# Kernel tuning notes

Hardware: AMD Instinct MI355X
Metric: run time of the kernel (lower is better)

The kernel has to match this reference:

```python
import jax, jax.numpy as jnp
import numpy as np

HEADS = 8
DIM_HEAD = 64
DIM = 512
KERNEL = 33
SCALE = DIM_HEAD ** -0.5


def setup_inputs() -> dict:
    key = jax.random.key(0)
    k1, k2, k3, k4, k5, k6 = jax.random.split(key, 6)
    b, n = 2, 2048
    inner = HEADS * DIM_HEAD
    x = jax.random.normal(k1, (b, n, DIM), dtype=jnp.float32)
    mask = jax.random.uniform(k2, (b, n)) < 0.9
    W_qkv = jax.random.normal(k3, (DIM, inner * 3), dtype=jnp.float32) / np.sqrt(DIM)
    W_out = jax.random.normal(k4, (inner, DIM), dtype=jnp.float32) / np.sqrt(inner)
    b_out = jax.random.normal(k5, (DIM,), dtype=jnp.float32) * 0.01
    # depthwise Conv2d(heads, heads, (K,1), groups=heads) weight: (O=heads, I/groups=1, K, 1)
    conv_w = jax.random.normal(k6, (HEADS, 1, KERNEL, 1), dtype=jnp.float32) / np.sqrt(KERNEL)
    return {"x": x, "mask": mask, "W_qkv": W_qkv, "W_out": W_out,
            "b_out": b_out, "conv_w": conv_w}


def reference(x, mask, W_qkv, W_out, b_out, conv_w):
    b, n, _ = x.shape
    h, d = HEADS, DIM_HEAD
    qkv = (x @ W_qkv).reshape(b, n, 3, h, d)          # chunk(3) then (h d) split
    q = qkv[:, :, 0].transpose(0, 2, 1, 3)            # b h n d
    k = qkv[:, :, 1].transpose(0, 2, 1, 3)
    v = qkv[:, :, 2].transpose(0, 2, 1, 3)
    dots = jnp.einsum('bhid,bhjd->bhij', q, k) * SCALE
    mask_value = -jnp.finfo(dots.dtype).max
    dots = jnp.where(mask[:, None, None, :], dots, mask_value)
    attn = jax.nn.softmax(dots, axis=-1)
    out = jnp.einsum('bhij,bhjd->bhid', attn, v)      # b h n d
    # depthwise residual conv over sequence axis (height), per head
    pad = KERNEL // 2
    res = jax.lax.conv_general_dilated(
        v, conv_w, window_strides=(1, 1), padding=((pad, pad), (0, 0)),
        dimension_numbers=('NCHW', 'OIHW', 'NCHW'), feature_group_count=h)
    out = out + res
    out = out.transpose(0, 2, 1, 3).reshape(b, n, h * d)  # b n (h d)
    out = out @ W_out + b_out
    out = jnp.where(mask[:, :, None], out, 0.0)
    return out
```

## Files before the change

kernel.cpp:

```cpp
#include <hip/hip_runtime.h>
#include <float.h>

#define BATCH 2
#define SEQ   2048
#define HEADS 8
#define DHEAD 64
#define DIMM  512
#define NQKV  1536
#define QSCALE_L2 (0.125f * 1.44269504f)

#define QKV_ELEMS ((size_t)BATCH * HEADS * SEQ * DHEAD)
#define BHS (BATCH * HEADS * SEQ)
#define NSPLIT 4

typedef __bf16 bf16x8 __attribute__((ext_vector_type(8)));
typedef short  s16x4  __attribute__((ext_vector_type(4)));
typedef float  f32x4  __attribute__((ext_vector_type(4)));

#if __has_builtin(__builtin_amdgcn_exp2f)
#define EXP2F __builtin_amdgcn_exp2f
#else
#define EXP2F exp2f
#endif

__device__ __forceinline__ unsigned short bfbits(float f) {
  __bf16 h = (__bf16)f;
  return *(unsigned short*)&h;
}
__device__ __forceinline__ float bf2f(unsigned short u) {
  return __uint_as_float((unsigned)u << 16);
}
__device__ __forceinline__ unsigned cvtpk(float a, float b) {
  unsigned r;
  asm("v_cvt_pk_bf16_f32 %0, %1, %2" : "=v"(r) : "v"(a), "v"(b));
  return r;
}
__device__ __forceinline__ f32x4 mfma16(s16x4 a, s16x4 b, f32x4 c) {
#if __has_builtin(__builtin_amdgcn_mfma_f32_16x16x16bf16_1k)
  return __builtin_amdgcn_mfma_f32_16x16x16bf16_1k(a, b, c, 0, 0, 0);
#else
  f32x4 d;
  asm("v_mfma_f32_16x16x16_bf16 %0, %1, %2, %3" : "=v"(d) : "v"(a), "v"(b), "v"(c));
  return d;
#endif
}

__device__ __forceinline__ void transpose_tile_dev(
    const float* __restrict__ W, unsigned short* __restrict__ Wt,
    int K, int N, int n0, int k0, int t, float T[64][65]) {
  {
    int r0 = t >> 4, c4 = t & 15;
#pragma unroll
    for (int rr = 0; rr < 4; ++rr) {
      int r = r0 + rr * 16;
      float4 v = *(const float4*)(W + (size_t)(k0 + r) * N + n0 + c4 * 4);
      T[r][c4 * 4 + 0] = v.x; T[r][c4 * 4 + 1] = v.y;
      T[r][c4 * 4 + 2] = v.z; T[r][c4 * 4 + 3] = v.w;
    }
  }
  __syncthreads();
  {
    int n = t >> 2, kc = t & 3;
    union { unsigned short u[16]; int4 v[2]; } p;
#pragma unroll
    for (int i = 0; i < 16; ++i) p.u[i] = bfbits(T[kc * 16 + i][n]);
    int4* dst = (int4*)(Wt + (size_t)(n0 + n) * K + k0 + kc * 16);
    dst[0] = p.v[0]; dst[1] = p.v[1];
  }
}

__global__ __launch_bounds__(256) void prep_all(
    const float* __restrict__ X, const void* __restrict__ mraw,
    const float* __restrict__ Wqkv, const float* __restrict__ Wout,
    unsigned short* __restrict__ Xbf, float* __restrict__ maskf,
    unsigned short* __restrict__ Wtq, unsigned short* __restrict__ Wto,
    unsigned* __restrict__ kmaxn) {
  __shared__ float T[64][65];
  __shared__ int f_bf16, f_f32, f_gt1, f_oddnz;
  const int b = blockIdx.x;
  const int t = threadIdx.x;
  if (b < 1024) {
    size_t i = ((size_t)b * 256 + t) * 8;
    float4 a0 = *(const float4*)(X + i);
    float4 a1 = *(const float4*)(X + i + 4);
    union { unsigned short u[8]; int4 v; } pk;
    pk.u[0] = bfbits(a0.x); pk.u[1] = bfbits(a0.y);
    pk.u[2] = bfbits(a0.z); pk.u[3] = bfbits(a0.w);
    pk.u[4] = bfbits(a1.x); pk.u[5] = bfbits(a1.y);
    pk.u[6] = bfbits(a1.z); pk.u[7] = bfbits(a1.w);
    *(int4*)(Xbf + i) = pk.v;
  } else if (b < 1216) {
    int bb2 = b - 1024;
    transpose_tile_dev(Wqkv, Wtq, DIMM, NQKV, (bb2 % 24) * 64, (bb2 / 24) * 64, t, T);
  } else if (b < 1280) {
    int bb2 = b - 1216;
    transpose_tile_dev(Wout, Wto, DIMM, DIMM, (bb2 & 7) * 64, (bb2 >> 3) * 64, t, T);
  } else {
    if (t < 16) kmaxn[t] = 0u;
    if (t == 0) { f_bf16 = 0; f_f32 = 0; f_gt1 = 0; f_oddnz = 0; }
    __syncthreads();
    const unsigned int* w = (const unsigned int*)mraw;
    unsigned int v = w[t];
    if (v == 0x3f803f80u) f_bf16 = 1;
    if (v == 0x3f800000u) f_f32 = 1;
    if (v > 1u)           f_gt1 = 1;
    if ((t & 1) && v != 0u) f_oddnz = 1;
    __syncthreads();
    int mode;
    if (f_bf16)       mode = 4;
    else if (f_f32)   mode = 3;
    else if (f_gt1)   mode = 1;
    else if (!f_oddnz) mode = 2;
    else              mode = 0;
    for (int i = t; i < BATCH * SEQ; i += 256) {
      bool keep;
      if (mode == 4)      keep = ((const unsigned short*)mraw)[i] != 0;
      else if (mode == 3) keep = ((const float*)mraw)[i] != 0.f;
      else if (mode == 1) keep = ((const unsigned char*)mraw)[i] != 0;
      else if (mode == 2) keep = w[2 * i] != 0u;
      else                keep = w[i] != 0u;
      maskf[i] = keep ? 1.f : 0.f;
    }
  }
}

__global__ __launch_bounds__(256) void gemm_qkv_mfma(
    const unsigned short* __restrict__ Xbf, const unsigned short* __restrict__ Wt,
    unsigned short* __restrict__ Qbf, unsigned short* __restrict__ Kbf,
    unsigned short* __restrict__ Vt, unsigned* __restrict__ kmaxn) {
  __shared__ __align__(16) unsigned char Al[128 * 128];
  __shared__ __align__(16) unsigned char Bl[64 * 128];
  const int tid = threadIdx.x;
  const int lane = tid & 63;
  const int w = tid >> 6;
  const int l15 = lane & 15, g = lane >> 4;
  const int wr = w >> 1, wc = w & 1;
  int bid = blockIdx.x;
  int lid = (bid & 7) * 96 + (bid >> 3);
  int by = lid / 24, bx = lid - by * 24;
  const int m0 = by * 128;

  f32x4 acc[4][2] = {};
  const int srow = tid >> 3, scg = tid & 7;
  const int rsw = (l15 & 7) << 4;

  for (int k0 = 0; k0 < DIMM; k0 += 64) {
    __syncthreads();
#pragma unroll
    for (int it = 0; it < 4; ++it) {
      int row = srow + it * 32;
      int sw = (row & 7) << 4;
      *(int4*)(Al + row * 128 + ((scg * 16) ^ sw)) =
          *(const int4*)(Xbf + (size_t)(m0 + row) * DIMM + k0 + scg * 8);
      if (it < 2) {
        *(int4*)(Bl + row * 128 + ((scg * 16) ^ sw)) =
            *(const int4*)(Wt + (size_t)(bx * 64 + row) * DIMM + k0 + scg * 8);
      }
    }
    __syncthreads();
#pragma unroll
    for (int ks = 0; ks < 2; ++ks) {
      bf16x8 af[4], bfr[2];
#pragma unroll
      for (int mi = 0; mi < 4; ++mi)
        af[mi] = *(const bf16x8*)(Al + (wr * 64 + mi * 16 + l15) * 128 +
                                  ((ks * 64 + g * 16) ^ rsw));
#pragma unroll
      for (int nj = 0; nj < 2; ++nj)
        bfr[nj] = *(const bf16x8*)(Bl + (wc * 32 + nj * 16 + l15) * 128 +
                                   ((ks * 64 + g * 16) ^ rsw));
#pragma unroll
      for (int mi = 0; mi < 4; ++mi)
#pragma unroll
        for (int nj = 0; nj < 2; ++nj)
          acc[mi][nj] = __builtin_amdgcn_mfma_f32_16x16x32_bf16(
              af[mi], bfr[nj], acc[mi][nj], 0, 0, 0);
    }
  }
  const int chunk = bx >> 3;
  const int bb = m0 >> 11;
  const int hh = bx & 7;
  if (chunk == 2) {
#pragma unroll
    for (int nj = 0; nj < 2; ++nj) {
      int dd = wc * 32 + nj * 16 + l15;
#pragma unroll
      for (int mi = 0; mi < 4; ++mi) {
        int ii0 = (m0 & (SEQ - 1)) + wr * 64 + mi * 16 + g * 4;
        union { unsigned short u[4]; ushort4 v; } pk;
#pragma unroll
        for (int r = 0; r < 4; ++r) pk.u[r] = bfbits(acc[mi][nj][r]);
        *(ushort4*)(Vt + ((size_t)(bb * HEADS + hh) * DHEAD + dd) * SEQ + ii0) = pk.v;
      }
    }
  } else {
    if (chunk == 1) {
      float kab = 0.f;
#pragma unroll
      for (int nj = 0; nj < 2; ++nj)
#pragma unroll
        for (int mi = 0; mi < 4; ++mi)
#pragma unroll
          for (int r = 0; r < 4; ++r) kab = fmaxf(kab, fabsf(acc[mi][nj][r]));
#pragma unroll
      for (int d = 1; d < 64; d <<= 1) kab = fmaxf(kab, __shfl_xor(kab, d));
      if (lane == 0)
        atomicMax(kmaxn + (bb * HEADS + hh), __float_as_uint(kab * 1.005f));
    }
    unsigned short* dst = (chunk == 0) ? Qbf : Kbf;
    const float sc = (chunk == 0) ? QSCALE_L2 : 1.f;
    __syncthreads();
#pragma unroll
    for (int nj = 0; nj < 2; ++nj) {
      int dd = wc * 32 + nj * 16 + l15;
#pragma unroll
      for (int mi = 0; mi < 4; ++mi) {
#pragma unroll
        for (int r = 0; r < 4; ++r) {
          int rowl = wr * 64 + mi * 16 + g * 4 + r;
          *(unsigned short*)(Al + rowl * 128 + ((dd * 2) ^ ((rowl & 7) << 4))) =
              bfbits(acc[mi][nj][r] * sc);
        }
      }
    }
    __syncthreads();
    const int rr = tid >> 1, hf = tid & 1;
    const int ii0 = (m0 & (SEQ - 1));
    unsigned short* gout =
        dst + ((size_t)(bb * HEADS + hh) * SEQ + ii0 + rr) * DHEAD + hf * 32;
    const int sw2 = (rr & 7) << 4;
#pragma unroll
    for (int q = 0; q < 4; ++q)
      *(int4*)(gout + q * 8) =
          *(const int4*)(Al + rr * 128 + ((hf * 64 + q * 16) ^ sw2));
  }
}

__global__ __launch_bounds__(256) void attn_split(const unsigned short* __restrict__ Qbf,
                                                  const unsigned short* __restrict__ Kbf,
                                                  const unsigned short* __restrict__ Vt,
                                                  const float* __restrict__ maskf,
                                                  const unsigned* __restrict__ kmaxn,
                                                  unsigned short* __restrict__ Po,
                                                  float* __restrict__ LSUM) {
  __shared__ __align__(16) unsigned char Ks[16384];
  __shared__ __align__(16) unsigned char Vs[16384];

  const int tid = threadIdx.x;
  const int lane = tid & 63;
  const int w = tid >> 6;
  const int l15 = lane & 15, g = lane >> 4;

  int fid = blockIdx.x;
  int lid = (fid & 7) * 128 + (fid >> 3);
  const int bh = lid >> 6;
  const int rem = lid & 63;
  const int qp = rem >> 2;
  const int quarter = rem & 3;
  const int bb = bh >> 3;

  const unsigned short* Qg = Qbf + ((size_t)bh * SEQ + qp * 128) * DHEAD;
  const unsigned short* Kg = Kbf + (size_t)bh * SEQ * DHEAD;
  const unsigned short* Vg = Vt  + (size_t)bh * DHEAD * SEQ;
  const float* mrow = maskf + bb * SEQ;

  bf16x8 qf0a, qf1a, qf0b, qf1b;
  {
    const unsigned char* qra = (const unsigned char*)(Qg + (size_t)(w * 16 + l15) * DHEAD);
    qf0a = *(const bf16x8*)(qra + g * 16);
    qf1a = *(const bf16x8*)(qra + 64 + g * 16);
    const unsigned char* qrb = qra + 64 * DHEAD * 2;
    qf0b = *(const bf16x8*)(qrb + g * 16);
    qf1b = *(const bf16x8*)(qrb + 64 + g * 16);
  }
  float Bxa, Bxb;
  {
    const float kabs = __uint_as_float(kmaxn[bh]);
    float qa = 0.f, qb2 = 0.f;
#pragma unroll
    for (int i = 0; i < 8; ++i) {
      float a0 = (float)qf0a[i]; qa += a0 * a0;
      float a1 = (float)qf1a[i]; qa += a1 * a1;
      float b0 = (float)qf0b[i]; qb2 += b0 * b0;
      float b1 = (float)qf1b[i]; qb2 += b1 * b1;
    }
    qa += __shfl_xor(qa, 16);  qa += __shfl_xor(qa, 32);
    qb2 += __shfl_xor(qb2, 16); qb2 += __shfl_xor(qb2, 32);
    Bxa = sqrtf(qa) * 8.f * kabs;
    Bxb = sqrtf(qb2) * 8.f * kabs;
  }

  f32x4 oa[4] = {}, ob[4] = {};
  float lsa = 0.f, lsb = 0.f;

  const int sm = tid >> 2;
  const int sc = (tid & 3) * 32;
  const int ssw = (sm & 7) << 4;
  const int vswap = (sm >> 3) & 1;
  const int rsw = (l15 & 7) << 4;
  const int vsw = rsw | (((l15 >> 3) & 1) << 3);
  const int kt0 = quarter * 8;

  int4 rk0, rk1, rv0, rv1;
  {
    const unsigned char* ksrc =
        (const unsigned char*)(Kg + (size_t)kt0 * 64 * DHEAD) + sm * 128 + sc;
    const unsigned char* vsrc =
        (const unsigned char*)(Vg + (size_t)sm * SEQ + kt0 * 64) + sc;
    rk0 = *(const int4*)(ksrc); rk1 = *(const int4*)(ksrc + 16);
    rv0 = *(const int4*)(vsrc); rv1 = *(const int4*)(vsrc + 16);
  }
  {
    *(int4*)(Ks + sm * 128 + ((sc)      ^ ssw)) = rk0;
    *(int4*)(Ks + sm * 128 + ((sc + 16) ^ ssw)) = rk1;
    int4 sv0 = vswap ? (int4){rv0.z, rv0.w, rv0.x, rv0.y} : rv0;
    int4 sv1 = vswap ? (int4){rv1.z, rv1.w, rv1.x, rv1.y} : rv1;
    *(int4*)(Vs + sm * 128 + ((sc)      ^ ssw)) = sv0;
    *(int4*)(Vs + sm * 128 + ((sc + 16) ^ ssw)) = sv1;
  }
  __syncthreads();

  for (int t = 0; t < 8; ++t) {
    const int kt = kt0 + t;
    const int co = (t & 1) << 13;
    const int no = co ^ 8192;
    float4 km[4];
#pragma unroll
    for (int j = 0; j < 4; ++j) km[j] = *(const float4*)(mrow + kt * 64 + 16 * j + 4 * g);
    if (t < 7) {
      const unsigned char* ksrc =
          (const unsigned char*)(Kg + (size_t)(kt + 1) * 64 * DHEAD) + sm * 128 + sc;
      const unsigned char* vsrc =
          (const unsigned char*)(Vg + (size_t)sm * SEQ + (kt + 1) * 64) + sc;
      rk0 = *(const int4*)(ksrc); rk1 = *(const int4*)(ksrc + 16);
      rv0 = *(const int4*)(vsrc); rv1 = *(const int4*)(vsrc + 16);
    }

    f32x4 sa[4], sb[4];
    __builtin_amdgcn_s_setprio(1);
#pragma unroll
    for (int j = 0; j < 4; ++j) {
      const unsigned char* krow = Ks + co + (16 * j + l15) * 128;
      bf16x8 kf0 = *(const bf16x8*)(krow + ((g * 16)      ^ rsw));
      bf16x8 kf1 = *(const bf16x8*)(krow + ((64 + g * 16) ^ rsw));
      f32x4 za = (f32x4){0.f, 0.f, 0.f, 0.f};
      za = __builtin_amdgcn_mfma_f32_16x16x32_bf16(kf0, qf0a, za, 0, 0, 0);
      za = __builtin_amdgcn_mfma_f32_16x16x32_bf16(kf1, qf1a, za, 0, 0, 0);
      sa[j] = za;
      f32x4 zb = (f32x4){0.f, 0.f, 0.f, 0.f};
      zb = __builtin_amdgcn_mfma_f32_16x16x32_bf16(kf0, qf0b, zb, 0, 0, 0);
      zb = __builtin_amdgcn_mfma_f32_16x16x32_bf16(kf1, qf1b, zb, 0, 0, 0);
      sb[j] = zb;
    }
    __builtin_amdgcn_s_setprio(0);

    s16x4 paA[4], paB[4];
#pragma unroll
    for (int j = 0; j < 4; ++j) {
      float a0 = EXP2F(sa[j][0] - Bxa) * km[j].x;
      float a1 = EXP2F(sa[j][1] - Bxa) * km[j].y;
      float a2 = EXP2F(sa[j][2] - Bxa) * km[j].z;
      float a3 = EXP2F(sa[j][3] - Bxa) * km[j].w;
      lsa += (a0 + a1) + (a2 + a3);
      union { uint2 u; s16x4 v; } pk;
      pk.u.x = cvtpk(a0, a1); pk.u.y = cvtpk(a2, a3);
      paA[j] = pk.v;
      float b0 = EXP2F(sb[j][0] - Bxb) * km[j].x;
      float b1 = EXP2F(sb[j][1] - Bxb) * km[j].y;
      float b2 = EXP2F(sb[j][2] - Bxb) * km[j].z;
      float b3 = EXP2F(sb[j][3] - Bxb) * km[j].w;
      lsb += (b0 + b1) + (b2 + b3);
      union { uint2 u; s16x4 v; } pk2;
      pk2.u.x = cvtpk(b0, b1); pk2.u.y = cvtpk(b2, b3);
      paB[j] = pk2.v;
    }

    __builtin_amdgcn_s_setprio(1);
#pragma unroll
    for (int dj = 0; dj < 4; ++dj) {
      const unsigned char* vrow = Vs + co + (16 * dj + l15) * 128;
#pragma unroll
      for (int j = 0; j < 4; ++j) {
        s16x4 vb = *(const s16x4*)(vrow + ((32 * j + 8 * g) ^ vsw));
        oa[dj] = mfma16(paA[j], vb, oa[dj]);
        ob[dj] = mfma16(paB[j], vb, ob[dj]);
      }
    }
    __builtin_amdgcn_s_setprio(0);

    if (t < 7) {
      *(int4*)(Ks + no + sm * 128 + ((sc)      ^ ssw)) = rk0;
      *(int4*)(Ks + no + sm * 128 + ((sc + 16) ^ ssw)) = rk1;
      int4 sv0 = vswap ? (int4){rv0.z, rv0.w, rv0.x, rv0.y} : rv0;
      int4 sv1 = vswap ? (int4){rv1.z, rv1.w, rv1.x, rv1.y} : rv1;
      *(int4*)(Vs + no + sm * 128 + ((sc)      ^ ssw)) = sv0;
      *(int4*)(Vs + no + sm * 128 + ((sc + 16) ^ ssw)) = sv1;
      __syncthreads();
    }
  }

#pragma unroll
  for (int r = 0; r < 4; ++r) {
    int rowa = qp * 128 + w * 16 + 4 * g + r;
    size_t basea = (size_t)quarter * QKV_ELEMS + ((size_t)bh * SEQ + rowa) * DHEAD + l15;
    Po[basea]      = bfbits(oa[0][r]);
    Po[basea + 16] = bfbits(oa[1][r]);
    Po[basea + 32] = bfbits(oa[2][r]);
    Po[basea + 48] = bfbits(oa[3][r]);
    size_t baseb = basea + (size_t)64 * DHEAD;
    Po[baseb]      = bfbits(ob[0][r]);
    Po[baseb + 16] = bfbits(ob[1][r]);
    Po[baseb + 32] = bfbits(ob[2][r]);
    Po[baseb + 48] = bfbits(ob[3][r]);
  }
  lsa += __shfl_xor(lsa, 16); lsa += __shfl_xor(lsa, 32);
  lsb += __shfl_xor(lsb, 16); lsb += __shfl_xor(lsb, 32);
  if (g == 0) {
    int rowa = qp * 128 + w * 16 + l15;
    LSUM[quarter * BHS + bh * SEQ + rowa] = lsa;
    LSUM[quarter * BHS + bh * SEQ + rowa + 64] = lsb;
  }
}

__global__ __launch_bounds__(256) void combine_conv(
    const unsigned short* __restrict__ Po, const float* __restrict__ LSUM,
    const unsigned short* __restrict__ Vt, const float* __restrict__ cw,
    unsigned short* __restrict__ Obf) {
  __shared__ float T[96][68];
  __shared__ float cwl[33];
  const int tid = threadIdx.x;
  const int bid = blockIdx.x;
  const int bh = bid >> 5;
  const int n0 = (bid & 31) * 64;
  const int hh = bh & 7;
  if (tid < 33) cwl[tid] = cw[hh * 33 + tid];
  for (int idx = tid; idx < 64 * 24; idx += 256) {
    int d = idx / 24, c4 = idx - (idx / 24) * 24;
    int nbase = n0 - 16 + c4 * 4;
    const unsigned short* src = Vt + ((size_t)bh * DHEAD + d) * SEQ;
#pragma unroll
    for (int q = 0; q < 4; ++q) {
      int n = nbase + q;
      T[c4 * 4 + q][d] = (n >= 0 && n < SEQ) ? bf2f(src[n]) : 0.f;
    }
  }
  __syncthreads();
#pragma unroll
  for (int p = 0; p < 4; ++p) {
    int n = (tid >> 4) + p * 16;
    int d4 = tid & 15;
    int row = bh * SEQ + n0 + n;
    float tot = 0.f;
#pragma unroll
    for (int q = 0; q < NSPLIT; ++q) tot += LSUM[q * BHS + row];
    float inv = (tot > 0.f) ? 1.f / tot : 0.f;
    float o0 = 0.f, o1 = 0.f, o2 = 0.f, o3 = 0.f;
#pragma unroll
    for (int q = 0; q < NSPLIT; ++q) {
      ushort4 a = *(const ushort4*)(Po + (size_t)q * QKV_ELEMS + (size_t)row * DHEAD + d4 * 4);
      o0 += bf2f(a.x); o1 += bf2f(a.y);
      o2 += bf2f(a.z); o3 += bf2f(a.w);
    }
    o0 *= inv; o1 *= inv; o2 *= inv; o3 *= inv;
#pragma unroll
    for (int t = 0; t < 33; ++t) {
      float wv = cwl[t];
      float4 tv = *(const float4*)&T[n + t][d4 * 4];
      o0 += wv * tv.x; o1 += wv * tv.y; o2 += wv * tv.z; o3 += wv * tv.w;
    }
    union { unsigned short u[4]; ushort4 v; } pk;
    pk.u[0] = bfbits(o0); pk.u[1] = bfbits(o1);
    pk.u[2] = bfbits(o2); pk.u[3] = bfbits(o3);
    *(ushort4*)(Obf + (size_t)row * DHEAD + d4 * 4) = pk.v;
  }
}

__global__ __launch_bounds__(256) void gemm_out_mfma(
    const unsigned short* __restrict__ Obf, const unsigned short* __restrict__ Wt,
    const float* __restrict__ bias, const float* __restrict__ maskf,
    float* __restrict__ out) {
  __shared__ __align__(16) unsigned char Al[64 * 128];
  __shared__ __align__(16) unsigned char Bl[64 * 128];
  const int tid = threadIdx.x;
  const int lane = tid & 63;
  const int w = tid >> 6;
  const int l15 = lane & 15, g = lane >> 4;
  const int wr = w >> 1, wc = w & 1;
  int bid = blockIdx.x;
  int lid = (bid & 7) * 64 + (bid >> 3);
  int by = lid >> 3, bx = lid & 7;
  const int m0 = by * 64, n0 = bx * 64;
  const int bb = m0 >> 11;
  const int ii0 = m0 & (SEQ - 1);

  f32x4 acc[2][2] = {};
  const int srow = tid >> 3, scg = tid & 7;
  const int rsw = (l15 & 7) << 4;

  for (int k0 = 0; k0 < DIMM; k0 += 64) {
    const int hh = k0 >> 6;
    __syncthreads();
#pragma unroll
    for (int it = 0; it < 2; ++it) {
      int row = srow + it * 32;
      int sw = (row & 7) << 4;
      *(int4*)(Al + row * 128 + ((scg * 16) ^ sw)) =
          *(const int4*)(Obf + ((size_t)(bb * HEADS + hh) * SEQ + ii0 + row) * DHEAD + scg * 8);
      *(int4*)(Bl + row * 128 + ((scg * 16) ^ sw)) =
          *(const int4*)(Wt + (size_t)(n0 + row) * DIMM + k0 + scg * 8);
    }
    __syncthreads();
#pragma unroll
    for (int ks = 0; ks < 2; ++ks) {
      bf16x8 af[2], bfr[2];
#pragma unroll
      for (int mi = 0; mi < 2; ++mi)
        af[mi] = *(const bf16x8*)(Al + (wr * 32 + mi * 16 + l15) * 128 +
                                  ((ks * 64 + g * 16) ^ rsw));
#pragma unroll
      for (int nj = 0; nj < 2; ++nj)
        bfr[nj] = *(const bf16x8*)(Bl + (wc * 32 + nj * 16 + l15) * 128 +
                                   ((ks * 64 + g * 16) ^ rsw));
#pragma unroll
      for (int mi = 0; mi < 2; ++mi)
#pragma unroll
        for (int nj = 0; nj < 2; ++nj)
          acc[mi][nj] = __builtin_amdgcn_mfma_f32_16x16x32_bf16(
              af[mi], bfr[nj], acc[mi][nj], 0, 0, 0);
    }
  }
#pragma unroll
  for (int nj = 0; nj < 2; ++nj) {
    int col = n0 + wc * 32 + nj * 16 + l15;
    float bcol = bias[col];
#pragma unroll
    for (int mi = 0; mi < 2; ++mi) {
#pragma unroll
      for (int r = 0; r < 4; ++r) {
        int m = m0 + wr * 32 + mi * 16 + g * 4 + r;
        out[(size_t)m * DIMM + col] = (acc[mi][nj][r] + bcol) * maskf[m];
      }
    }
  }
}

extern "C" void kernel_launch(void* const* d_in, const int* in_sizes, int n_in,
                              void* d_out, int out_size, void* d_ws, size_t ws_size,
                              hipStream_t stream) {
  const float* x     = (const float*)d_in[0];
  const void*  mask  = d_in[1];
  const float* Wqkv  = (const float*)d_in[2];
  const float* Wout  = (const float*)d_in[3];
  const float* bout  = (const float*)d_in[4];
  const float* convw = (const float*)d_in[5];
  float* out = (float*)d_out;

  float* maskf = (float*)d_ws;
  unsigned* kmaxn = (unsigned*)(maskf + 4096);
  unsigned short* Qbf = (unsigned short*)(kmaxn + 64);
  unsigned short* Kbf = Qbf + QKV_ELEMS;
  unsigned short* Vt  = Kbf + QKV_ELEMS;
  unsigned short* Po  = Vt + QKV_ELEMS;
  float* LSUM         = (float*)(Po + NSPLIT * QKV_ELEMS);
  unsigned short* Obf = (unsigned short*)(LSUM + NSPLIT * BHS);
  unsigned short* Wtq = Obf + QKV_ELEMS;
  unsigned short* Wto = Wtq + (size_t)NQKV * DIMM;
  unsigned short* Xbf = Wto + (size_t)DIMM * DIMM;

  prep_all<<<1281, 256, 0, stream>>>(x, mask, Wqkv, Wout, Xbf, maskf, Wtq, Wto, kmaxn);
  gemm_qkv_mfma<<<768, 256, 0, stream>>>(Xbf, Wtq, Qbf, Kbf, Vt, kmaxn);
  attn_split<<<1024, 256, 0, stream>>>(Qbf, Kbf, Vt, maskf, kmaxn, Po, LSUM);
  combine_conv<<<512, 256, 0, stream>>>(Po, LSUM, Vt, convw, Obf);
  gemm_out_mfma<<<512, 256, 0, stream>>>(Obf, Wto, bout, maskf, out);
}
```

Measured before the change: 99.45 us.

## Fuse X bf16 conversion into QKV GEMM and use K=32 MFMA for PV

```diff
diff --git a/kernel.cpp b/kernel.cpp
--- a/kernel.cpp
+++ b/kernel.cpp
@@ -14,7 +14,6 @@
 #define NSPLIT 4
 
 typedef __bf16 bf16x8 __attribute__((ext_vector_type(8)));
-typedef short  s16x4  __attribute__((ext_vector_type(4)));
 typedef float  f32x4  __attribute__((ext_vector_type(4)));
 
 #if __has_builtin(__builtin_amdgcn_exp2f)
@@ -35,15 +34,6 @@
   asm("v_cvt_pk_bf16_f32 %0, %1, %2" : "=v"(r) : "v"(a), "v"(b));
   return r;
 }
-__device__ __forceinline__ f32x4 mfma16(s16x4 a, s16x4 b, f32x4 c) {
-#if __has_builtin(__builtin_amdgcn_mfma_f32_16x16x16bf16_1k)
-  return __builtin_amdgcn_mfma_f32_16x16x16bf16_1k(a, b, c, 0, 0, 0);
-#else
-  f32x4 d;
-  asm("v_mfma_f32_16x16x16_bf16 %0, %1, %2, %3" : "=v"(d) : "v"(a), "v"(b), "v"(c));
-  return d;
-#endif
-}
 
 __device__ __forceinline__ void transpose_tile_dev(
     const float* __restrict__ W, unsigned short* __restrict__ Wt,
@@ -70,31 +60,20 @@
 }
 
 __global__ __launch_bounds__(256) void prep_all(
-    const float* __restrict__ X, const void* __restrict__ mraw,
+    const void* __restrict__ mraw,
     const float* __restrict__ Wqkv, const float* __restrict__ Wout,
-    unsigned short* __restrict__ Xbf, float* __restrict__ maskf,
+    float* __restrict__ maskf,
     unsigned short* __restrict__ Wtq, unsigned short* __restrict__ Wto,
     unsigned* __restrict__ kmaxn) {
   __shared__ float T[64][65];
   __shared__ int f_bf16, f_f32, f_gt1, f_oddnz;
   const int b = blockIdx.x;
   const int t = threadIdx.x;
-  if (b < 1024) {
-    size_t i = ((size_t)b * 256 + t) * 8;
-    float4 a0 = *(const float4*)(X + i);
-    float4 a1 = *(const float4*)(X + i + 4);
-    union { unsigned short u[8]; int4 v; } pk;
-    pk.u[0] = bfbits(a0.x); pk.u[1] = bfbits(a0.y);
-    pk.u[2] = bfbits(a0.z); pk.u[3] = bfbits(a0.w);
-    pk.u[4] = bfbits(a1.x); pk.u[5] = bfbits(a1.y);
-    pk.u[6] = bfbits(a1.z); pk.u[7] = bfbits(a1.w);
-    *(int4*)(Xbf + i) = pk.v;
-  } else if (b < 1216) {
-    int bb2 = b - 1024;
-    transpose_tile_dev(Wqkv, Wtq, DIMM, NQKV, (bb2 % 24) * 64, (bb2 / 24) * 64, t, T);
-  } else if (b < 1280) {
-    int bb2 = b - 1216;
-    transpose_tile_dev(Wout, Wto, DIMM, DIMM, (bb2 & 7) * 64, (bb2 >> 3) * 64, t, T);
+  if (b < 192) {
+    transpose_tile_dev(Wqkv, Wtq, DIMM, NQKV, (b % 24) * 64, (b / 24) * 64, t, T);
+  } else if (b < 256) {
+    int c = b - 192;
+    transpose_tile_dev(Wout, Wto, DIMM, DIMM, (c & 7) * 64, (c >> 3) * 64, t, T);
   } else {
     if (t < 16) kmaxn[t] = 0u;
     if (t == 0) { f_bf16 = 0; f_f32 = 0; f_gt1 = 0; f_oddnz = 0; }
@@ -125,7 +104,7 @@
 }
 
 __global__ __launch_bounds__(256) void gemm_qkv_mfma(
-    const unsigned short* __restrict__ Xbf, const unsigned short* __restrict__ Wt,
+    const float* __restrict__ X, const unsigned short* __restrict__ Wt,
     unsigned short* __restrict__ Qbf, unsigned short* __restrict__ Kbf,
     unsigned short* __restrict__ Vt, unsigned* __restrict__ kmaxn) {
   __shared__ __align__(16) unsigned char Al[128 * 128];
@@ -150,8 +129,15 @@
     for (int it = 0; it < 4; ++it) {
       int row = srow + it * 32;
       int sw = (row & 7) << 4;
-      *(int4*)(Al + row * 128 + ((scg * 16) ^ sw)) =
-          *(const int4*)(Xbf + (size_t)(m0 + row) * DIMM + k0 + scg * 8);
+      const float* asrc = X + (size_t)(m0 + row) * DIMM + k0 + scg * 8;
+      float4 a0 = *(const float4*)asrc;
+      float4 a1 = *(const float4*)(asrc + 4);
+      union { unsigned short u[8]; int4 v; } pk;
+      pk.u[0] = bfbits(a0.x); pk.u[1] = bfbits(a0.y);
+      pk.u[2] = bfbits(a0.z); pk.u[3] = bfbits(a0.w);
+      pk.u[4] = bfbits(a1.x); pk.u[5] = bfbits(a1.y);
+      pk.u[6] = bfbits(a1.z); pk.u[7] = bfbits(a1.w);
+      *(int4*)(Al + row * 128 + ((scg * 16) ^ sw)) = pk.v;
       if (it < 2) {
         *(int4*)(Bl + row * 128 + ((scg * 16) ^ sw)) =
             *(const int4*)(Wt + (size_t)(bx * 64 + row) * DIMM + k0 + scg * 8);
@@ -245,6 +231,7 @@
                                                   float* __restrict__ LSUM) {
   __shared__ __align__(16) unsigned char Ks[16384];
   __shared__ __align__(16) unsigned char Vs[16384];
+  __shared__ __align__(16) unsigned char Ps[8192];
 
   const int tid = threadIdx.x;
   const int lane = tid & 63;
@@ -296,10 +283,9 @@
   const int sm = tid >> 2;
   const int sc = (tid & 3) * 32;
   const int ssw = (sm & 7) << 4;
-  const int vswap = (sm >> 3) & 1;
   const int rsw = (l15 & 7) << 4;
-  const int vsw = rsw | (((l15 >> 3) & 1) << 3);
   const int kt0 = quarter * 8;
+  unsigned char* Pw = Ps + w * 2048 + l15 * 128;
 
   int4 rk0, rk1, rv0, rv1;
   {
@@ -310,14 +296,10 @@
     rk0 = *(const int4*)(ksrc); rk1 = *(const int4*)(ksrc + 16);
     rv0 = *(const int4*)(vsrc); rv1 = *(const int4*)(vsrc + 16);
   }
-  {
-    *(int4*)(Ks + sm * 128 + ((sc)      ^ ssw)) = rk0;
-    *(int4*)(Ks + sm * 128 + ((sc + 16) ^ ssw)) = rk1;
-    int4 sv0 = vswap ? (int4){rv0.z, rv0.w, rv0.x, rv0.y} : rv0;
-    int4 sv1 = vswap ? (int4){rv1.z, rv1.w, rv1.x, rv1.y} : rv1;
-    *(int4*)(Vs + sm * 128 + ((sc)      ^ ssw)) = sv0;
-    *(int4*)(Vs + sm * 128 + ((sc + 16) ^ ssw)) = sv1;
-  }
+  *(int4*)(Ks + sm * 128 + ((sc)      ^ ssw)) = rk0;
+  *(int4*)(Ks + sm * 128 + ((sc + 16) ^ ssw)) = rk1;
+  *(int4*)(Vs + sm * 128 + ((sc)      ^ ssw)) = rv0;
+  *(int4*)(Vs + sm * 128 + ((sc + 16) ^ ssw)) = rv1;
   __syncthreads();
 
   for (int t = 0; t < 8; ++t) {
@@ -354,47 +336,68 @@
     }
     __builtin_amdgcn_s_setprio(0);
 
-    s16x4 paA[4], paB[4];
-#pragma unroll
-    for (int j = 0; j < 4; ++j) {
-      float a0 = EXP2F(sa[j][0] - Bxa) * km[j].x;
-      float a1 = EXP2F(sa[j][1] - Bxa) * km[j].y;
-      float a2 = EXP2F(sa[j][2] - Bxa) * km[j].z;
-      float a3 = EXP2F(sa[j][3] - Bxa) * km[j].w;
-      lsa += (a0 + a1) + (a2 + a3);
-      union { uint2 u; s16x4 v; } pk;
-      pk.u.x = cvtpk(a0, a1); pk.u.y = cvtpk(a2, a3);
-      paA[j] = pk.v;
-      float b0 = EXP2F(sb[j][0] - Bxb) * km[j].x;
-      float b1 = EXP2F(sb[j][1] - Bxb) * km[j].y;
-      float b2 = EXP2F(sb[j][2] - Bxb) * km[j].z;
-      float b3 = EXP2F(sb[j][3] - Bxb) * km[j].w;
-      lsb += (b0 + b1) + (b2 + b3);
-      union { uint2 u; s16x4 v; } pk2;
-      pk2.u.x = cvtpk(b0, b1); pk2.u.y = cvtpk(b2, b3);
-      paB[j] = pk2.v;
-    }
-
-    __builtin_amdgcn_s_setprio(1);
-#pragma unroll
-    for (int dj = 0; dj < 4; ++dj) {
-      const unsigned char* vrow = Vs + co + (16 * dj + l15) * 128;
+    {
+      uint2 pk[4];
 #pragma unroll
       for (int j = 0; j < 4; ++j) {
-        s16x4 vb = *(const s16x4*)(vrow + ((32 * j + 8 * g) ^ vsw));
-        oa[dj] = mfma16(paA[j], vb, oa[dj]);
-        ob[dj] = mfma16(paB[j], vb, ob[dj]);
-      }
-    }
-    __builtin_amdgcn_s_setprio(0);
+        float p0 = EXP2F(sa[j][0] - Bxa) * km[j].x;
+        float p1 = EXP2F(sa[j][1] - Bxa) * km[j].y;
+        float p2 = EXP2F(sa[j][2] - Bxa) * km[j].z;
+        float p3 = EXP2F(sa[j][3] - Bxa) * km[j].w;
+        lsa += (p0 + p1) + (p2 + p3);
+        pk[j].x = cvtpk(p0, p1);
+        pk[j].y = cvtpk(p2, p3);
+      }
+#pragma unroll
+      for (int j = 0; j < 4; ++j)
+        *(uint2*)(Pw + ((32 * j + 8 * g) ^ rsw)) = pk[j];
+      bf16x8 paf0 = *(const bf16x8*)(Pw + ((16 * g)      ^ rsw));
+      bf16x8 paf1 = *(const bf16x8*)(Pw + ((64 + 16 * g) ^ rsw));
+      __builtin_amdgcn_s_setprio(1);
+#pragma unroll
+      for (int dj = 0; dj < 4; ++dj) {
+        const unsigned char* vrow = Vs + co + (16 * dj + l15) * 128;
+        bf16x8 vb0 = *(const bf16x8*)(vrow + ((16 * g)      ^ rsw));
+        bf16x8 vb1 = *(const bf16x8*)(vrow + ((64 + 16 * g) ^ rsw));
+        oa[dj] = __builtin_amdgcn_mfma_f32_16x16x32_bf16(paf0, vb0, oa[dj], 0, 0, 0);
+        oa[dj] = __builtin_amdgcn_mfma_f32_16x16x32_bf16(paf1, vb1, oa[dj], 0, 0, 0);
+      }
+      __builtin_amdgcn_s_setprio(0);
+    }
+    {
+      uint2 pk[4];
+#pragma unroll
+      for (int j = 0; j < 4; ++j) {
+        float p0 = EXP2F(sb[j][0] - Bxb) * km[j].x;
+        float p1 = EXP2F(sb[j][1] - Bxb) * km[j].y;
+        float p2 = EXP2F(sb[j][2] - Bxb) * km[j].z;
+        float p3 = EXP2F(sb[j][3] - Bxb) * km[j].w;
+        lsb += (p0 + p1) + (p2 + p3);
+        pk[j].x = cvtpk(p0, p1);
+        pk[j].y = cvtpk(p2, p3);
+      }
+#pragma unroll
+      for (int j = 0; j < 4; ++j)
+        *(uint2*)(Pw + ((32 * j + 8 * g) ^ rsw)) = pk[j];
+      bf16x8 paf0 = *(const bf16x8*)(Pw + ((16 * g)      ^ rsw));
+      bf16x8 paf1 = *(const bf16x8*)(Pw + ((64 + 16 * g) ^ rsw));
+      __builtin_amdgcn_s_setprio(1);
+#pragma unroll
+      for (int dj = 0; dj < 4; ++dj) {
+        const unsigned char* vrow = Vs + co + (16 * dj + l15) * 128;
+        bf16x8 vb0 = *(const bf16x8*)(vrow + ((16 * g)      ^ rsw));
+        bf16x8 vb1 = *(const bf16x8*)(vrow + ((64 + 16 * g) ^ rsw));
+        ob[dj] = __builtin_amdgcn_mfma_f32_16x16x32_bf16(paf0, vb0, ob[dj], 0, 0, 0);
+        ob[dj] = __builtin_amdgcn_mfma_f32_16x16x32_bf16(paf1, vb1, ob[dj], 0, 0, 0);
+      }
+      __builtin_amdgcn_s_setprio(0);
+    }
 
     if (t < 7) {
       *(int4*)(Ks + no + sm * 128 + ((sc)      ^ ssw)) = rk0;
       *(int4*)(Ks + no + sm * 128 + ((sc + 16) ^ ssw)) = rk1;
-      int4 sv0 = vswap ? (int4){rv0.z, rv0.w, rv0.x, rv0.y} : rv0;
-      int4 sv1 = vswap ? (int4){rv1.z, rv1.w, rv1.x, rv1.y} : rv1;
-      *(int4*)(Vs + no + sm * 128 + ((sc)      ^ ssw)) = sv0;
-      *(int4*)(Vs + no + sm * 128 + ((sc + 16) ^ ssw)) = sv1;
+      *(int4*)(Vs + no + sm * 128 + ((sc)      ^ ssw)) = rv0;
+      *(int4*)(Vs + no + sm * 128 + ((sc + 16) ^ ssw)) = rv1;
       __syncthreads();
     }
   }
@@ -565,10 +568,9 @@
   unsigned short* Obf = (unsigned short*)(LSUM + NSPLIT * BHS);
   unsigned short* Wtq = Obf + QKV_ELEMS;
   unsigned short* Wto = Wtq + (size_t)NQKV * DIMM;
-  unsigned short* Xbf = Wto + (size_t)DIMM * DIMM;
-
-  prep_all<<<1281, 256, 0, stream>>>(x, mask, Wqkv, Wout, Xbf, maskf, Wtq, Wto, kmaxn);
-  gemm_qkv_mfma<<<768, 256, 0, stream>>>(Xbf, Wtq, Qbf, Kbf, Vt, kmaxn);
+
+  prep_all<<<257, 256, 0, stream>>>(mask, Wqkv, Wout, maskf, Wtq, Wto, kmaxn);
+  gemm_qkv_mfma<<<768, 256, 0, stream>>>(x, Wtq, Qbf, Kbf, Vt, kmaxn);
   attn_split<<<1024, 256, 0, stream>>>(Qbf, Kbf, Vt, maskf, kmaxn, Po, LSUM);
   combine_conv<<<512, 256, 0, stream>>>(Po, LSUM, Vt, convw, Obf);
   gemm_out_mfma<<<512, 256, 0, stream>>>(Obf, Wto, bout, maskf, out);
```

Measured after the change: 104.2 us. 4.8% more time.
